# Kernel tuning notes

Measured on AMD Instinct MI355X. Metric: run time of the kernel, lower is better.

The kernel has to match this reference:

```python
import jax, jax.numpy as jnp
import numpy as np

U, I, D = 50000, 25000, 128          # users, items, emb_size
E = 1_000_000                        # user-item interactions
L = 3                                # num_layers
B = 4096                             # BPR batch size
N = U + I                            # total graph nodes


def setup_inputs() -> dict:
    key = jax.random.key(0)
    k1, k2, k3, k4, k5, k6, k7 = jax.random.split(key, 7)
    # Xavier-ish embedding tables
    user_emb = jax.random.normal(k1, (U, D), jnp.float32) * 0.1
    item_emb = jax.random.normal(k2, (I, D), jnp.float32) * 0.1
    # random bipartite interactions -> symmetric COO adjacency over N nodes
    eu = jax.random.randint(k3, (E,), 0, U)            # user node ids
    ei = jax.random.randint(k4, (E,), 0, I) + U        # item node ids (offset)
    adj_row = jnp.concatenate([eu, ei]).astype(jnp.int32)   # [2E]
    adj_col = jnp.concatenate([ei, eu]).astype(jnp.int32)   # [2E]
    # symmetric normalization D^-1/2 A D^-1/2 (matches create_adj_mat)
    deg = jax.ops.segment_sum(jnp.ones(2 * E, jnp.float32), adj_row, num_segments=N)
    d_inv = jnp.where(deg > 0, deg ** -0.5, 0.0)
    adj_vals = d_inv[adj_row] * d_inv[adj_col]               # [2E] float32
    users = jax.random.randint(k5, (B,), 0, U).astype(jnp.int32)
    pos_items = jax.random.randint(k6, (B,), 0, I).astype(jnp.int32)
    neg_items = jax.random.randint(k7, (B,), 0, I).astype(jnp.int32)
    return dict(user_emb=user_emb, item_emb=item_emb, adj_row=adj_row,
                adj_col=adj_col, adj_vals=adj_vals, users=users,
                pos_items=pos_items, neg_items=neg_items)


def _spmm(vals, row, col, x):
    # sparse [N,N] @ dense [N,D] via gather + segment_sum
    return jax.ops.segment_sum(vals[:, None] * x[col], row, num_segments=N)


def reference(user_emb, item_emb, adj_row, adj_col, adj_vals,
              users, pos_items, neg_items):
    ego = jnp.concatenate([user_emb, item_emb], axis=0)      # [N, D]
    # FAITHFUL to the torch source: ego_embeddings is never reassigned inside
    # the layer loop, so every one of the L layer outputs equals A @ ego.
    # mean(stack([ego, A@ego, ..., A@ego])) == (ego + L * A@ego) / (L + 1)
    h = _spmm(adj_vals, adj_row, adj_col, ego)               # [N, D]
    final = (ego + L * h) / (L + 1)                          # mean over L+1 layers
    u_final = final[:U]
    i_final = final[U:]
    u_g = u_final[users]                                     # [B, D]
    pos_i_g = i_final[pos_items]                             # [B, D]
    neg_i_g = i_final[neg_items]                             # [B, D]
    return (u_g, pos_i_g, neg_i_g, i_final)
```

## Files before the change

### kernel.cpp

```cpp
#include <hip/hip_runtime.h>
#include <hip/hip_bf16.h>

#define U_CNT 50000
#define I_CNT 25000
#define D_DIM 128
#define E_CNT 1000000
#define B_CNT 4096
#define ICAP 96
#define UCAP 64
#define PNCAP 16
#define BM_WORDS 1600
#define IRANGE (I_CNT / 8)
#define URANGE (U_CNT / 8)
#define NGROUP 1000
#define CHUNK  (E_CNT / NGROUP)
#define BUCKET_BLKS (NGROUP * 8)
#define CVT_BLKS 3125


__device__ __forceinline__ unsigned pack_bf2(float lo, float hi) {
    __hip_bfloat16 a = __float2bfloat16(lo);
    __hip_bfloat16 b = __float2bfloat16(hi);
    unsigned short ua = *reinterpret_cast<unsigned short*>(&a);
    unsigned short ub = *reinterpret_cast<unsigned short*>(&b);
    return ((unsigned)ub << 16) | ua;
}
__device__ __forceinline__ float bf_lo(unsigned w) { return __uint_as_float(w << 16); }
__device__ __forceinline__ float bf_hi(unsigned w) { return __uint_as_float(w & 0xffff0000u); }

__global__ __launch_bounds__(256) void prep_kernel(
        const int* __restrict__ users,
        const int* __restrict__ pos_items,
        const int* __restrict__ neg_items,
        unsigned*  __restrict__ bitmap,
        int*       __restrict__ slot,
        int*       __restrict__ pncnt,
        int*       __restrict__ pnbuck) {
    const int i = blockIdx.x * blockDim.x + threadIdx.x;
    if (i < B_CNT) {
        const int u = users[i];
        atomicOr(&bitmap[u >> 5], 1u << (u & 31));
        atomicCAS(&slot[u], 0, i + 1);
    }
    if (i < 2 * B_CNT) {
        const int idx = (i < B_CNT) ? pos_items[i] : neg_items[i - B_CNT];
        const int c = atomicAdd(&pncnt[idx], 1);
        if (c < PNCAP) pnbuck[idx * PNCAP + c] = B_CNT + i;
    }
}

__global__ __launch_bounds__(256) void bucket_cvt_kernel(
        const int*      __restrict__ adj_row,
        const int*      __restrict__ adj_col,
        const float*    __restrict__ adj_vals,
        const float*    __restrict__ user_emb,
        const unsigned* __restrict__ bitmap,
        const int*      __restrict__ slot,
        int*  __restrict__ icnt,  int*  __restrict__ ucnt,
        int2* __restrict__ ibuck, int2* __restrict__ ubuck,
        unsigned* __restrict__ ue16) {
    if (blockIdx.x < BUCKET_BLKS) {
        const unsigned x = blockIdx.x & 7;
        const int      g = blockIdx.x >> 3;
        const int base = g * CHUNK + (int)threadIdx.x * 4;
        if (base >= g * CHUNK + CHUNK) return;

        const int4   uu = *(const int4*)  (adj_row  + base);
        const int4   tt = *(const int4*)  (adj_col  + base);
        const float4 vv = *(const float4*)(adj_vals + base);
        const unsigned us[4] = {(unsigned)uu.x, (unsigned)uu.y,
                                (unsigned)uu.z, (unsigned)uu.w};
        const unsigned ts[4] = {(unsigned)(tt.x - U_CNT), (unsigned)(tt.y - U_CNT),
                                (unsigned)(tt.z - U_CNT), (unsigned)(tt.w - U_CNT)};
        const float    vs[4] = {vv.x, vv.y, vv.z, vv.w};
#pragma unroll
        for (int k = 0; k < 4; ++k) {
            const unsigned u = us[k], t = ts[k];
            const int vb = __float_as_int(vs[k]);
            if (t / IRANGE == x) {
                const int c = atomicAdd(&icnt[t], 1);
                ibuck[(size_t)t * ICAP + c] = make_int2((int)u, vb);
            }
            if (u / URANGE == x) {
                if ((bitmap[u >> 5] >> (u & 31)) & 1u) {
                    const int j0 = slot[u] - 1;
                    const int c2 = atomicAdd(&ucnt[j0], 1);
                    ubuck[(size_t)j0 * UCAP + c2] = make_int2((int)t, vb);
                }
            }
        }
    } else {
        const int bid = blockIdx.x - BUCKET_BLKS;
        int i = bid * 1024 + threadIdx.x;
#pragma unroll
        for (int r = 0; r < 4; ++r, i += 256) {
            const float2 f = ((const float2*)user_emb)[i];
            ue16[i] = pack_bf2(f.x, f.y);
        }
    }
}

__global__ __launch_bounds__(256) void gather_kernel(
        const float*    __restrict__ user_emb,
        const float*    __restrict__ item_emb,
        const unsigned* __restrict__ ue16,
        const int*      __restrict__ users,
        const int*      __restrict__ slot,
        const int*      __restrict__ icnt,
        const int*      __restrict__ ucnt,
        const int*      __restrict__ pncnt,
        const int*      __restrict__ pnbuck,
        const int2*     __restrict__ ibuck,
        const int2*     __restrict__ ubuck,
        float*          __restrict__ out) {
    const int lane = threadIdx.x & 63;
    const int w    = (blockIdx.x * blockDim.x + threadIdx.x) >> 6;

    if (w < I_CNT) {
        const int t   = w;
        const int n   = min(icnt[t], ICAP);
        const int2* b = ibuck + (size_t)t * ICAP;
        const int sub = lane >> 4;
        const int cl  = lane & 15;
        float a0=0.f,a1=0.f,a2=0.f,a3=0.f,a4=0.f,a5=0.f,a6=0.f,a7=0.f;

        int q = 0;
        for (; q + 8 <= n; q += 8) {
            const int2 eA = b[q + sub];
            const int2 eB = b[q + 4 + sub];
            const uint4 wA = *(const uint4*)(ue16 + (size_t)eA.x * 64 + cl * 4);
            const uint4 wB = *(const uint4*)(ue16 + (size_t)eB.x * 64 + cl * 4);
            const float vA = __int_as_float(eA.y), vB = __int_as_float(eB.y);
            a0 += vA*bf_lo(wA.x) + vB*bf_lo(wB.x);
            a1 += vA*bf_hi(wA.x) + vB*bf_hi(wB.x);
            a2 += vA*bf_lo(wA.y) + vB*bf_lo(wB.y);
            a3 += vA*bf_hi(wA.y) + vB*bf_hi(wB.y);
            a4 += vA*bf_lo(wA.z) + vB*bf_lo(wB.z);
            a5 += vA*bf_hi(wA.z) + vB*bf_hi(wB.z);
            a6 += vA*bf_lo(wA.w) + vB*bf_lo(wB.w);
            a7 += vA*bf_hi(wA.w) + vB*bf_hi(wB.w);
        }
        if (q + 4 <= n) {
            const int2 e = b[q + sub];
            const uint4 wv = *(const uint4*)(ue16 + (size_t)e.x * 64 + cl * 4);
            const float v = __int_as_float(e.y);
            a0 += v*bf_lo(wv.x); a1 += v*bf_hi(wv.x);
            a2 += v*bf_lo(wv.y); a3 += v*bf_hi(wv.y);
            a4 += v*bf_lo(wv.z); a5 += v*bf_hi(wv.z);
            a6 += v*bf_lo(wv.w); a7 += v*bf_hi(wv.w);
            q += 4;
        }
        if (q < n) {
            const int r = q + sub;
            if (r < n) {
                const int2 e = b[r];
                const uint4 wv = *(const uint4*)(ue16 + (size_t)e.x * 64 + cl * 4);
                const float v = __int_as_float(e.y);
                a0 += v*bf_lo(wv.x); a1 += v*bf_hi(wv.x);
                a2 += v*bf_lo(wv.y); a3 += v*bf_hi(wv.y);
                a4 += v*bf_lo(wv.z); a5 += v*bf_hi(wv.z);
                a6 += v*bf_lo(wv.w); a7 += v*bf_hi(wv.w);
            }
        }
        a0 += __shfl_xor(a0, 16); a0 += __shfl_xor(a0, 32);
        a1 += __shfl_xor(a1, 16); a1 += __shfl_xor(a1, 32);
        a2 += __shfl_xor(a2, 16); a2 += __shfl_xor(a2, 32);
        a3 += __shfl_xor(a3, 16); a3 += __shfl_xor(a3, 32);
        a4 += __shfl_xor(a4, 16); a4 += __shfl_xor(a4, 32);
        a5 += __shfl_xor(a5, 16); a5 += __shfl_xor(a5, 32);
        a6 += __shfl_xor(a6, 16); a6 += __shfl_xor(a6, 32);
        a7 += __shfl_xor(a7, 16); a7 += __shfl_xor(a7, 32);

        if (sub == 0) {
            const float* ie = item_emb + (size_t)t * D_DIM + cl * 8;
            const float4 g0 = *(const float4*)(ie);
            const float4 g1 = *(const float4*)(ie + 4);
            float4 o0, o1;
            o0.x = (g0.x + 3.0f*a0)*0.25f; o0.y = (g0.y + 3.0f*a1)*0.25f;
            o0.z = (g0.z + 3.0f*a2)*0.25f; o0.w = (g0.w + 3.0f*a3)*0.25f;
            o1.x = (g1.x + 3.0f*a4)*0.25f; o1.y = (g1.y + 3.0f*a5)*0.25f;
            o1.z = (g1.z + 3.0f*a6)*0.25f; o1.w = (g1.w + 3.0f*a7)*0.25f;
            float* orow = out + (size_t)(3 * B_CNT + t) * D_DIM + cl * 8;
            *(float4*)orow = o0; *(float4*)(orow + 4) = o1;
            const int pn = min(pncnt[t], PNCAP);
            for (int c = 0; c < pn; ++c) {
                const int row = pnbuck[t * PNCAP + c];
                float* pr = out + (size_t)row * D_DIM + cl * 8;
                *(float4*)pr = o0; *(float4*)(pr + 4) = o1;
            }
        }
    } else if (w < I_CNT + B_CNT) {
        const int j  = w - I_CNT;
        const int u  = users[j];
        const int j0 = slot[u] - 1;
        const int n  = min(ucnt[j0], UCAP);
        const int2* b = ubuck + (size_t)j0 * UCAP;
        float ax = 0.0f, ay = 0.0f;
        int q = 0;
        for (; q + 4 <= n; q += 4) {
            const int2 e0 = b[q], e1 = b[q+1], e2 = b[q+2], e3 = b[q+3];
            const float2 x0 = ((const float2*)(item_emb + (size_t)e0.x * D_DIM))[lane];
            const float2 x1 = ((const float2*)(item_emb + (size_t)e1.x * D_DIM))[lane];
            const float2 x2 = ((const float2*)(item_emb + (size_t)e2.x * D_DIM))[lane];
            const float2 x3 = ((const float2*)(item_emb + (size_t)e3.x * D_DIM))[lane];
            const float v0 = __int_as_float(e0.y), v1 = __int_as_float(e1.y);
            const float v2 = __int_as_float(e2.y), v3 = __int_as_float(e3.y);
            ax += v0*x0.x + v1*x1.x + v2*x2.x + v3*x3.x;
            ay += v0*x0.y + v1*x1.y + v2*x2.y + v3*x3.y;
        }
        for (; q < n; ++q) {
            const int2 e = b[q];
            const float2 xx = ((const float2*)(item_emb + (size_t)e.x * D_DIM))[lane];
            const float v = __int_as_float(e.y);
            ax += v * xx.x;
            ay += v * xx.y;
        }
        const float2 eg = ((const float2*)(user_emb + (size_t)u * D_DIM))[lane];
        float2 o;
        o.x = (eg.x + 3.0f * ax) * 0.25f;
        o.y = (eg.y + 3.0f * ay) * 0.25f;
        ((float2*)(out + (size_t)j * D_DIM))[lane] = o;
    }
}

extern "C" void kernel_launch(void* const* d_in, const int* in_sizes, int n_in,
                              void* d_out, int out_size, void* d_ws, size_t ws_size,
                              hipStream_t stream) {
    const float* user_emb  = (const float*)d_in[0];
    const float* item_emb  = (const float*)d_in[1];
    const int*   adj_row   = (const int*)  d_in[2];
    const int*   adj_col   = (const int*)  d_in[3];
    const float* adj_vals  = (const float*)d_in[4];
    const int*   users     = (const int*)  d_in[5];
    const int*   pos_items = (const int*)  d_in[6];
    const int*   neg_items = (const int*)  d_in[7];
    float* out = (float*)d_out;

    unsigned* bitmap = (unsigned*)d_ws;
    int* slot  = (int*)(bitmap + BM_WORDS);
    int* icnt  = slot + U_CNT;
    int* ucnt  = icnt + I_CNT;
    int* pncnt = ucnt + B_CNT;
    int2* ibuck = (int2*)(pncnt + I_CNT);
    int2* ubuck = ibuck + (size_t)I_CNT * ICAP;
    int*  pnbuck = (int*)(ubuck + (size_t)B_CNT * UCAP);
    unsigned* ue16 = (unsigned*)(pnbuck + (size_t)I_CNT * PNCAP);

    const size_t zero_ints = BM_WORDS + U_CNT + I_CNT + B_CNT + I_CNT;
    hipMemsetAsync(bitmap, 0, zero_ints * sizeof(int), stream);

    prep_kernel<<<(2 * B_CNT + 255) / 256, 256, 0, stream>>>(
        users, pos_items, neg_items, bitmap, slot, pncnt, pnbuck);

    bucket_cvt_kernel<<<BUCKET_BLKS + CVT_BLKS, 256, 0, stream>>>(
        adj_row, adj_col, adj_vals, user_emb, bitmap, slot,
        icnt, ucnt, ibuck, ubuck, ue16);

    gather_kernel<<<((I_CNT + B_CNT) * 64 + 255) / 256, 256, 0, stream>>>(
        user_emb, item_emb, ue16, users, slot, icnt, ucnt,
        pncnt, pnbuck, ibuck, ubuck, out);
}
```

Baseline: 203.0 us.

## Add nontemporal streaming loads/stores and interleave item-gather blocks across ranges

Streaming reads of the COO arrays, user embeddings and item embeddings, plus the output writes, now use nontemporal loads and stores so they do not evict the reused bf16 user table and buckets from cache. The gather kernel's item blocks are remapped so consecutive blocks cycle through the eight item ranges (blockIdx & 7), matching the bucket kernel's interleaving. The intent is to spread work across memory channels and XCDs and improve L2 locality. Nontemporal hints may behave differently on this hardware, and the new mapping launches a few extra blocks that exit early.

```diff
diff --git a/kernel.cpp b/kernel.cpp
--- a/kernel.cpp
+++ b/kernel.cpp
@@ -16,6 +16,13 @@
 #define CHUNK  (E_CNT / NGROUP)
 #define BUCKET_BLKS (NGROUP * 8)
 #define CVT_BLKS 3125
+#define GI_BLKS (8 * 782)
+#define GU_BLKS (B_CNT / 4)
+
+typedef int    vi4 __attribute__((ext_vector_type(4)));
+typedef float  vf4 __attribute__((ext_vector_type(4)));
+typedef float  vf2 __attribute__((ext_vector_type(2)));
+typedef unsigned vu4 __attribute__((ext_vector_type(4)));
 
 
 __device__ __forceinline__ unsigned pack_bf2(float lo, float hi) {
@@ -65,9 +72,9 @@
         const int base = g * CHUNK + (int)threadIdx.x * 4;
         if (base >= g * CHUNK + CHUNK) return;
 
-        const int4   uu = *(const int4*)  (adj_row  + base);
-        const int4   tt = *(const int4*)  (adj_col  + base);
-        const float4 vv = *(const float4*)(adj_vals + base);
+        const vi4 uu = __builtin_nontemporal_load((const vi4*)(adj_row  + base));
+        const vi4 tt = __builtin_nontemporal_load((const vi4*)(adj_col  + base));
+        const vf4 vv = __builtin_nontemporal_load((const vf4*)(adj_vals + base));
         const unsigned us[4] = {(unsigned)uu.x, (unsigned)uu.y,
                                 (unsigned)uu.z, (unsigned)uu.w};
         const unsigned ts[4] = {(unsigned)(tt.x - U_CNT), (unsigned)(tt.y - U_CNT),
@@ -94,8 +101,8 @@
         int i = bid * 1024 + threadIdx.x;
 #pragma unroll
         for (int r = 0; r < 4; ++r, i += 256) {
-            const float2 f = ((const float2*)user_emb)[i];
-            ue16[i] = pack_bf2(f.x, f.y);
+            const vf2 f = __builtin_nontemporal_load(((const vf2*)user_emb) + i);
+            __builtin_nontemporal_store(pack_bf2(f.x, f.y), ue16 + i);
         }
     }
 }
@@ -114,10 +121,15 @@
         const int2*     __restrict__ ubuck,
         float*          __restrict__ out) {
     const int lane = threadIdx.x & 63;
-    const int w    = (blockIdx.x * blockDim.x + threadIdx.x) >> 6;
-
-    if (w < I_CNT) {
-        const int t   = w;
+    const int wib  = threadIdx.x >> 6;
+
+    if (blockIdx.x < GI_BLKS) {
+        const int x  = blockIdx.x & 7;
+        const int g  = blockIdx.x >> 3;
+        const int li = g * 4 + wib;
+        if (li >= IRANGE) return;
+        const int t = x * IRANGE + li;
+
         const int n   = min(icnt[t], ICAP);
         const int2* b = ibuck + (size_t)t * ICAP;
         const int sub = lane >> 4;
@@ -128,8 +140,8 @@
         for (; q + 8 <= n; q += 8) {
             const int2 eA = b[q + sub];
             const int2 eB = b[q + 4 + sub];
-            const uint4 wA = *(const uint4*)(ue16 + (size_t)eA.x * 64 + cl * 4);
-            const uint4 wB = *(const uint4*)(ue16 + (size_t)eB.x * 64 + cl * 4);
+            const vu4 wA = *(const vu4*)(ue16 + (size_t)eA.x * 64 + cl * 4);
+            const vu4 wB = *(const vu4*)(ue16 + (size_t)eB.x * 64 + cl * 4);
             const float vA = __int_as_float(eA.y), vB = __int_as_float(eB.y);
             a0 += vA*bf_lo(wA.x) + vB*bf_lo(wB.x);
             a1 += vA*bf_hi(wA.x) + vB*bf_hi(wB.x);
@@ -142,7 +154,7 @@
         }
         if (q + 4 <= n) {
             const int2 e = b[q + sub];
-            const uint4 wv = *(const uint4*)(ue16 + (size_t)e.x * 64 + cl * 4);
+            const vu4 wv = *(const vu4*)(ue16 + (size_t)e.x * 64 + cl * 4);
             const float v = __int_as_float(e.y);
             a0 += v*bf_lo(wv.x); a1 += v*bf_hi(wv.x);
             a2 += v*bf_lo(wv.y); a3 += v*bf_hi(wv.y);
@@ -154,7 +166,7 @@
             const int r = q + sub;
             if (r < n) {
                 const int2 e = b[r];
-                const uint4 wv = *(const uint4*)(ue16 + (size_t)e.x * 64 + cl * 4);
+                const vu4 wv = *(const vu4*)(ue16 + (size_t)e.x * 64 + cl * 4);
                 const float v = __int_as_float(e.y);
                 a0 += v*bf_lo(wv.x); a1 += v*bf_hi(wv.x);
                 a2 += v*bf_lo(wv.y); a3 += v*bf_hi(wv.y);
@@ -173,24 +185,26 @@
 
         if (sub == 0) {
             const float* ie = item_emb + (size_t)t * D_DIM + cl * 8;
-            const float4 g0 = *(const float4*)(ie);
-            const float4 g1 = *(const float4*)(ie + 4);
-            float4 o0, o1;
+            const vf4 g0 = __builtin_nontemporal_load((const vf4*)ie);
+            const vf4 g1 = __builtin_nontemporal_load((const vf4*)(ie + 4));
+            vf4 o0, o1;
             o0.x = (g0.x + 3.0f*a0)*0.25f; o0.y = (g0.y + 3.0f*a1)*0.25f;
             o0.z = (g0.z + 3.0f*a2)*0.25f; o0.w = (g0.w + 3.0f*a3)*0.25f;
             o1.x = (g1.x + 3.0f*a4)*0.25f; o1.y = (g1.y + 3.0f*a5)*0.25f;
             o1.z = (g1.z + 3.0f*a6)*0.25f; o1.w = (g1.w + 3.0f*a7)*0.25f;
             float* orow = out + (size_t)(3 * B_CNT + t) * D_DIM + cl * 8;
-            *(float4*)orow = o0; *(float4*)(orow + 4) = o1;
+            __builtin_nontemporal_store(o0, (vf4*)orow);
+            __builtin_nontemporal_store(o1, (vf4*)(orow + 4));
             const int pn = min(pncnt[t], PNCAP);
             for (int c = 0; c < pn; ++c) {
                 const int row = pnbuck[t * PNCAP + c];
                 float* pr = out + (size_t)row * D_DIM + cl * 8;
-                *(float4*)pr = o0; *(float4*)(pr + 4) = o1;
-            }
-        }
-    } else if (w < I_CNT + B_CNT) {
-        const int j  = w - I_CNT;
+                __builtin_nontemporal_store(o0, (vf4*)pr);
+                __builtin_nontemporal_store(o1, (vf4*)(pr + 4));
+            }
+        }
+    } else {
+        const int j = (blockIdx.x - GI_BLKS) * 4 + wib;
         const int u  = users[j];
         const int j0 = slot[u] - 1;
         const int n  = min(ucnt[j0], UCAP);
@@ -256,7 +270,7 @@
         adj_row, adj_col, adj_vals, user_emb, bitmap, slot,
         icnt, ucnt, ibuck, ubuck, ue16);
 
-    gather_kernel<<<((I_CNT + B_CNT) * 64 + 255) / 256, 256, 0, stream>>>(
+    gather_kernel<<<GI_BLKS + GU_BLKS, 256, 0, stream>>>(
         user_emb, item_emb, ue16, users, slot, icnt, ucnt,
         pncnt, pnbuck, ibuck, ubuck, out);
 }
```

After: 206.1 us. No clear change (+1.5%).
